# Optimization experiments

Hardware: AMD Instinct MI355X
Metric: run time of the kernel (lower is better)

## Reference

```python
import jax, jax.numpy as jnp
import numpy as np
from jax import lax

KERNELS = (3, 5, 7, 9, 11, 13, 15)
H = W = 4096


def _box_mean(x, k):
    """2D box-mean filter with replicate (edge) padding, computed separably.

    Edge padding is separable, so (pad2d -> kxk box) == (padH -> kx1 box -> padW -> 1xk box).
    x: [N, 1, H, W]
    """
    p = k // 2
    kh = jnp.full((1, 1, k, 1), 1.0 / k, dtype=x.dtype)
    kw = jnp.full((1, 1, 1, k), 1.0 / k, dtype=x.dtype)
    dn = ('NCHW', 'OIHW', 'NCHW')
    y = jnp.pad(x, ((0, 0), (0, 0), (p, p), (0, 0)), mode='edge')
    y = lax.conv_general_dilated(y, kh, (1, 1), 'VALID', dimension_numbers=dn)
    y = jnp.pad(y, ((0, 0), (0, 0), (0, 0), (p, p)), mode='edge')
    y = lax.conv_general_dilated(y, kw, (1, 1), 'VALID', dimension_numbers=dn)
    return y


def setup_inputs() -> dict:
    key = jax.random.key(0)
    k1, k2 = jax.random.split(key)
    x = jax.random.uniform(k1, (1, 1, H, W), dtype=jnp.float32)
    # binary occupancy-style map, as float (torch uses mapU8 -> fp16 multiply)
    map_mask = (jax.random.uniform(k2, (H, W)) > 0.5).astype(jnp.float32)
    return {"x": x, "map_mask": map_mask}


def reference(x, map_mask):
    # sum of 7 multi-scale box means, averaged, then masked by the map
    acc = _box_mean(x, KERNELS[0])
    for k in KERNELS[1:]:
        acc = acc + _box_mean(x, k)
    out = acc / len(KERNELS)
    return out * map_mask[None, None, :, :]
```

## Files before the change

kernel.cpp:

```cpp
#include <hip/hip_runtime.h>


#define TILE  64
#define HALO  7
#define LW    (TILE + 2 * HALO)
#define PROWS (LW + 1)
#define PSTR  81
#define HH    4096
#define WW    4096

__global__ __launch_bounds__(256) void meanconv_kernel(
    const float* __restrict__ x, const float* __restrict__ mask,
    float* __restrict__ out)
{
    __shared__ float P[PROWS * PSTR];
    const int tid = threadIdx.x;
    const int c0  = blockIdx.x * TILE;
    const int r0  = blockIdx.y * TILE;

    for (int idx = tid; idx < LW * LW; idx += 256) {
        int lr = idx / LW, lc = idx - lr * LW;
        int gr = r0 + lr - HALO; gr = min(max(gr, 0), HH - 1);
        int gc = c0 + lc - HALO; gc = min(max(gc, 0), WW - 1);
        P[(lr + 1) * PSTR + (lc + 1)] = x[gr * WW + gc];
    }
    if (tid < PROWS) P[tid * PSTR] = 0.0f;
    if (tid >= 128 && tid < 128 + LW + 1) P[tid - 128] = 0.0f;
    __syncthreads();

    if (tid < LW) {
        float run = 0.0f;
        const int base = (tid + 1) * PSTR;
        #pragma unroll 6
        for (int c = 1; c <= LW; ++c) { run += P[base + c]; P[base + c] = run; }
    }
    __syncthreads();

    if (tid < LW) {
        float run = 0.0f;
        const int c = tid + 1;
        #pragma unroll 6
        for (int r = 1; r <= LW; ++r) { run += P[r * PSTR + c]; P[r * PSTR + c] = run; }
    }
    __syncthreads();

    const int tx = tid & 63;
    const int ty = tid >> 6;
    for (int rr = ty; rr < TILE; rr += 4) {
        const int A = rr + HALO;
        const int B = tx + HALO;
        float acc = 0.0f;
        #pragma unroll
        for (int p = 1; p <= 7; ++p) {
            const int k = 2 * p + 1;
            const float w = 1.0f / (7.0f * (float)(k * k));
            const float s = P[(A + p + 1) * PSTR + (B + p + 1)]
                          - P[(A - p)     * PSTR + (B + p + 1)]
                          - P[(A + p + 1) * PSTR + (B - p)]
                          + P[(A - p)     * PSTR + (B - p)];
            acc += w * s;
        }
        const int gr = r0 + rr, gc = c0 + tx;
        out[gr * WW + gc] = acc * mask[gr * WW + gc];
    }
}

extern "C" void kernel_launch(void* const* d_in, const int* in_sizes, int n_in,
                              void* d_out, int out_size, void* d_ws, size_t ws_size,
                              hipStream_t stream) {
    const float* x    = (const float*)d_in[0];
    const float* mask = (const float*)d_in[1];
    float*       out  = (float*)d_out;
    dim3 grid(WW / TILE, HH / TILE);
    meanconv_kernel<<<grid, 256, 0, stream>>>(x, mask, out);
}
```

Measured before the change: 188.6 us.

## Parallelize prefix sums across lanes and vectorize tile loads and output stores

The tile load now uses float4 global reads for interior tiles and fuses the row prefix sum into the load. Each row is split into four 20-element segments combined with a shuffle scan. The column scan is split the same way, so up to 320 threads work on it instead of 78. The output stage computes 8 contiguous pixels per thread and uses float4 mask loads and output stores. The halo is widened to 8 on the left for alignment, and the serial scan phases that left most threads idle are replaced, at the cost of more registers and strided LDS access.

```diff
diff --git a/kernel.cpp b/kernel.cpp
--- a/kernel.cpp
+++ b/kernel.cpp
@@ -1,67 +1,117 @@
 #include <hip/hip_runtime.h>
 
 
-#define TILE  64
-#define HALO  7
-#define LW    (TILE + 2 * HALO)
-#define PROWS (LW + 1)
-#define PSTR  81
-#define HH    4096
-#define WW    4096
+#define TILE   64
+#define HALO   7
+#define LHX    8
+#define NCOL   80
+#define NROW   78
+#define PSTR   83
+#define PROWSA 81
+#define HH     4096
+#define WW     4096
 
 __global__ __launch_bounds__(256) void meanconv_kernel(
     const float* __restrict__ x, const float* __restrict__ mask,
     float* __restrict__ out)
 {
-    __shared__ float P[PROWS * PSTR];
+    __shared__ float P[PROWSA * PSTR];
     const int tid = threadIdx.x;
     const int c0  = blockIdx.x * TILE;
     const int r0  = blockIdx.y * TILE;
 
-    for (int idx = tid; idx < LW * LW; idx += 256) {
-        int lr = idx / LW, lc = idx - lr * LW;
-        int gr = r0 + lr - HALO; gr = min(max(gr, 0), HH - 1);
-        int gc = c0 + lc - HALO; gc = min(max(gc, 0), WW - 1);
-        P[(lr + 1) * PSTR + (lc + 1)] = x[gr * WW + gc];
-    }
-    if (tid < PROWS) P[tid * PSTR] = 0.0f;
-    if (tid >= 128 && tid < 128 + LW + 1) P[tid - 128] = 0.0f;
-    __syncthreads();
+    if (tid < 81) P[tid] = 0.0f;
 
-    if (tid < LW) {
-        float run = 0.0f;
-        const int base = (tid + 1) * PSTR;
-        #pragma unroll 6
-        for (int c = 1; c <= LW; ++c) { run += P[base + c]; P[base + c] = run; }
+    const bool xint = (c0 >= LHX) && (c0 - LHX + NCOL <= WW);
+
+    for (int idx = tid; idx < NROW * 4; idx += 256) {
+        const int lr  = idx >> 2;
+        const int s   = idx & 3;
+        const int gr  = min(max(r0 + lr - HALO, 0), HH - 1);
+        const int gc0 = c0 - LHX + 20 * s;
+        float v[20];
+        if (xint) {
+            const float* src = &x[(size_t)gr * WW + gc0];
+            #pragma unroll
+            for (int q = 0; q < 5; ++q) {
+                const float4 t = *(const float4*)(src + 4 * q);
+                v[4*q+0] = t.x; v[4*q+1] = t.y; v[4*q+2] = t.z; v[4*q+3] = t.w;
+            }
+        } else {
+            #pragma unroll
+            for (int i = 0; i < 20; ++i) {
+                const int gc = min(max(gc0 + i, 0), WW - 1);
+                v[i] = x[(size_t)gr * WW + gc];
+            }
+        }
+        #pragma unroll
+        for (int i = 1; i < 20; ++i) v[i] += v[i - 1];
+        const float tot = v[19];
+        float sum = tot;
+        float u = __shfl_up(sum, 1, 4); if (s >= 1) sum += u;
+        u       = __shfl_up(sum, 2, 4); if (s >= 2) sum += u;
+        const float off = sum - tot;
+        float* dst = &P[(lr + 1) * PSTR + 1 + 20 * s];
+        #pragma unroll
+        for (int i = 0; i < 20; ++i) dst[i] = v[i] + off;
     }
     __syncthreads();
 
-    if (tid < LW) {
+    for (int idx = tid; idx < 80 * 4; idx += 256) {
+        const int c  = (idx >> 2) + 1;
+        const int s  = idx & 3;
+        const int rs = 1 + 20 * s;
+        float v[20];
         float run = 0.0f;
-        const int c = tid + 1;
-        #pragma unroll 6
-        for (int r = 1; r <= LW; ++r) { run += P[r * PSTR + c]; P[r * PSTR + c] = run; }
+        #pragma unroll
+        for (int i = 0; i < 20; ++i) {
+            const int r = rs + i;
+            float t = P[r * PSTR + c];
+            t = (r < 79) ? t : 0.0f;
+            run += t; v[i] = run;
+        }
+        const float tot = run;
+        float sum = tot;
+        float u = __shfl_up(sum, 1, 4); if (s >= 1) sum += u;
+        u       = __shfl_up(sum, 2, 4); if (s >= 2) sum += u;
+        const float off = sum - tot;
+        #pragma unroll
+        for (int i = 0; i < 20; ++i) {
+            const int r = rs + i;
+            if (r < 79) P[r * PSTR + c] = v[i] + off;
+        }
     }
     __syncthreads();
 
-    const int tx = tid & 63;
-    const int ty = tid >> 6;
-    for (int rr = ty; rr < TILE; rr += 4) {
-        const int A = rr + HALO;
-        const int B = tx + HALO;
-        float acc = 0.0f;
+    const int g  = tid & 7;
+    const int ty = tid >> 3;
+    const int B0 = 8 * g;
+    #pragma unroll
+    for (int j = 0; j < 2; ++j) {
+        const int rr = ty + 32 * j;
+        const int A  = rr + HALO;
+        float a[8] = {0.f,0.f,0.f,0.f,0.f,0.f,0.f,0.f};
         #pragma unroll
         for (int p = 1; p <= 7; ++p) {
-            const int k = 2 * p + 1;
+            const int   k = 2 * p + 1;
             const float w = 1.0f / (7.0f * (float)(k * k));
-            const float s = P[(A + p + 1) * PSTR + (B + p + 1)]
-                          - P[(A - p)     * PSTR + (B + p + 1)]
-                          - P[(A + p + 1) * PSTR + (B - p)]
-                          + P[(A - p)     * PSTR + (B - p)];
-            acc += w * s;
+            const float* rT = &P[(A - p) * PSTR];
+            const float* rB = &P[(A + p + 1) * PSTR];
+            const int cl = B0 + LHX - p;
+            const int cr = cl + 2 * p + 1;
+            #pragma unroll
+            for (int i = 0; i < 8; ++i) {
+                a[i] += w * (rB[cr + i] - rT[cr + i] - rB[cl + i] + rT[cl + i]);
+            }
         }
-        const int gr = r0 + rr, gc = c0 + tx;
-        out[gr * WW + gc] = acc * mask[gr * WW + gc];
+        const int gr = r0 + rr, gc = c0 + B0;
+        const float4 m0 = *(const float4*)&mask[(size_t)gr * WW + gc];
+        const float4 m1 = *(const float4*)&mask[(size_t)gr * WW + gc + 4];
+        float4 o0, o1;
+        o0.x = a[0] * m0.x; o0.y = a[1] * m0.y; o0.z = a[2] * m0.z; o0.w = a[3] * m0.w;
+        o1.x = a[4] * m1.x; o1.y = a[5] * m1.y; o1.z = a[6] * m1.z; o1.w = a[7] * m1.w;
+        *(float4*)&out[(size_t)gr * WW + gc]     = o0;
+        *(float4*)&out[(size_t)gr * WW + gc + 4] = o1;
     }
 }
 
```

Result: faster. 184.0 us (-2.4%).
